# Kernel tuning notes

Measured on AMD Instinct MI355X. Metric: run time of the kernel, lower is better.

## Reference

```python
import jax, jax.numpy as jnp
import numpy as np

N_PTS = 2_000_000
N_VOX = 500_000
N_EMB = 1_000_000
EMBED_DIM = 16


def _interp_offset():
    # 8 corners of the unit cube, same order as torch.meshgrid([0,1]*3) -> reshape(-1,3)
    o = jnp.array([0.0, 1.0], dtype=jnp.float32)
    return jnp.stack(jnp.meshgrid(o, o, o, indexing='ij'), axis=-1).reshape(-1, 3)  # [8,3]


def setup_inputs() -> dict:
    key = jax.random.key(0)
    k1, k2, k3, k4, k5 = jax.random.split(key, 5)
    pts = jax.random.uniform(k1, (N_PTS, 3), dtype=jnp.float32)
    p2v_idx = jax.random.randint(k2, (N_PTS,), 0, N_VOX, dtype=jnp.int64 if jax.config.jax_enable_x64 else jnp.int32)
    embeddings = jax.random.normal(k3, (N_EMB, EMBED_DIM), dtype=jnp.float32) * (EMBED_DIM ** -0.5)
    center_points = jax.random.uniform(k4, (N_VOX, 3), dtype=jnp.float32)
    center2corner = jax.random.randint(k5, (N_VOX, 8), 0, N_EMB, dtype=jnp.int64 if jax.config.jax_enable_x64 else jnp.int32)
    voxel_size = jnp.ones((1,), dtype=jnp.float32)
    return {"pts": pts, "p2v_idx": p2v_idx, "embeddings": embeddings,
            "center_points": center_points, "center2corner": center2corner,
            "voxel_size": voxel_size}


def reference(pts, p2v_idx, embeddings, center_points, center2corner, voxel_size):
    offset = _interp_offset()                      # [8,3]
    cp = center_points[p2v_idx]                    # [N,3]   gather voxel centers
    cidx = center2corner[p2v_idx]                  # [N,8]   gather corner indices
    emb = embeddings[cidx]                         # [N,8,D] gather corner embeddings
    # relative position inside voxel, in [0,1]
    p = (pts - cp) / voxel_size + 0.5              # [N,3]
    p = p[:, None, :]                              # [N,1,3]
    # trilinear weights: prod over xyz of (p if corner==1 else 1-p)
    r = jnp.prod(p * offset + (1.0 - p) * (1.0 - offset), axis=-1)  # [N,8]
    return jnp.einsum('nc,ncd->nd', r, emb)        # [N,D]
```

## Files before the change

kernel.cpp:

```cpp
#include <hip/hip_runtime.h>


typedef float v4f __attribute__((ext_vector_type(4)));


__global__ void k_init_gbase(unsigned* __restrict__ gbase, int NB, unsigned CAP) {
    int i = blockIdx.x * blockDim.x + threadIdx.x;
    if (i < NB) gbase[i] = (unsigned)i * CAP;
}

__global__ __launch_bounds__(1024) void k_bucket(
    const int*   __restrict__ p2v,
    const float* __restrict__ pts,
    unsigned*    __restrict__ gbase,
    unsigned*    __restrict__ vA,
    v4f*         __restrict__ recA,
    int N, int NB)
{
    __shared__ unsigned cnt[512];
    __shared__ unsigned cur[512];
    const int tid = threadIdx.x;
    const int i0 = (blockIdx.x * 1024 + tid) * 8;

    for (int b = tid; b < NB; b += 1024) cnt[b] = 0u;
    __syncthreads();

    int vv[8];
    const bool full = (i0 + 7 < N);
    if (full) {
        const int4 a = *(const int4*)(p2v + i0);
        const int4 b4 = *(const int4*)(p2v + i0 + 4);
        vv[0]=a.x; vv[1]=a.y; vv[2]=a.z; vv[3]=a.w;
        vv[4]=b4.x; vv[5]=b4.y; vv[6]=b4.z; vv[7]=b4.w;
        #pragma unroll
        for (int k = 0; k < 8; ++k) atomicAdd(&cnt[vv[k] >> 11], 1u);
    } else {
        for (int k = 0; k < 8; ++k)
            if (i0 + k < N) { vv[k] = p2v[i0 + k]; atomicAdd(&cnt[vv[k] >> 11], 1u); }
    }
    __syncthreads();

    for (int b = tid; b < NB; b += 1024) {
        const unsigned c = cnt[b];
        cur[b] = c ? atomicAdd(&gbase[b], c) : 0u;
    }
    __syncthreads();

    if (full) {
        const v4f* p4 = (const v4f*)pts;
        const size_t fb = (size_t)3 * (size_t)(i0 >> 2);
        const v4f f0 = p4[fb], f1 = p4[fb+1], f2 = p4[fb+2];
        const v4f f3 = p4[fb+3], f4 = p4[fb+4], f5 = p4[fb+5];
        const float xs[8] = {f0.x, f0.w, f1.z, f2.y, f3.x, f3.w, f4.z, f5.y};
        const float ys[8] = {f0.y, f1.x, f1.w, f2.z, f3.y, f4.x, f4.w, f5.z};
        const float zs[8] = {f0.z, f1.y, f2.x, f2.w, f3.z, f4.y, f5.x, f5.w};
        #pragma unroll
        for (int k = 0; k < 8; ++k) {
            const unsigned pos = atomicAdd(&cur[vv[k] >> 11], 1u);
            v4f r; r.x = xs[k]; r.y = ys[k]; r.z = zs[k]; r.w = __int_as_float(i0 + k);
            recA[pos] = r;
            vA[pos] = (unsigned)vv[k];
        }
    } else {
        for (int k = 0; k < 8; ++k) {
            const int i = i0 + k;
            if (i >= N) break;
            const unsigned pos = atomicAdd(&cur[vv[k] >> 11], 1u);
            v4f r;
            r.x = pts[3*(size_t)i]; r.y = pts[3*(size_t)i+1]; r.z = pts[3*(size_t)i+2];
            r.w = __int_as_float(i);
            recA[pos] = r;
            vA[pos] = (unsigned)vv[k];
        }
    }
}

__global__ __launch_bounds__(256) void k_scan_nb(const unsigned* __restrict__ gbase,
                                                 unsigned* __restrict__ bo,
                                                 int NB, unsigned CAP) {
    __shared__ unsigned tsum[256];
    const int tid = threadIdx.x;
    const int i0 = tid * 2;
    const unsigned c0 = (i0     < NB) ? gbase[i0]     - (unsigned)i0       * CAP : 0u;
    const unsigned c1 = (i0 + 1 < NB) ? gbase[i0 + 1] - (unsigned)(i0 + 1) * CAP : 0u;
    tsum[tid] = c0 + c1; __syncthreads();
    for (int off = 1; off < 256; off <<= 1) {
        unsigned x = tsum[tid];
        unsigned y = (tid >= off) ? tsum[tid - off] : 0u;
        __syncthreads();
        tsum[tid] = x + y;
        __syncthreads();
    }
    const unsigned prefix = (tid > 0) ? tsum[tid - 1] : 0u;
    if (i0     < NB) bo[i0]     = prefix;
    if (i0 + 1 < NB) bo[i0 + 1] = prefix + c0;
}

__global__ __launch_bounds__(1024) void k_binsort(
    const unsigned* __restrict__ gbase,
    const unsigned* __restrict__ bo,
    const unsigned* __restrict__ vA,
    const v4f*      __restrict__ recA,
    unsigned*       __restrict__ vsort,
    v4f*            __restrict__ rec,
    unsigned CAP)
{
    __shared__ unsigned h[2048];
    __shared__ unsigned tsum[1024];
    const int b   = blockIdx.x;
    const int tid = threadIdx.x;
    const unsigned in0   = (unsigned)b * CAP;
    const unsigned cntb  = gbase[b] - in0;
    const unsigned obase = bo[b];
    const unsigned vbase = (unsigned)b << 11;

    h[tid] = 0u; h[tid + 1024] = 0u;
    __syncthreads();

    for (unsigned j = tid; j < cntb; j += 1024)
        atomicAdd(&h[vA[in0 + j] - vbase], 1u);
    __syncthreads();

    const unsigned a0 = h[2 * tid];
    const unsigned a1 = h[2 * tid + 1];
    tsum[tid] = a0 + a1; __syncthreads();
    for (int off = 1; off < 1024; off <<= 1) {
        unsigned x = tsum[tid];
        unsigned y = (tid >= off) ? tsum[tid - off] : 0u;
        __syncthreads();
        tsum[tid] = x + y;
        __syncthreads();
    }
    const unsigned pre = (tid > 0) ? tsum[tid - 1] : 0u;
    h[2 * tid]     = pre;
    h[2 * tid + 1] = pre + a0;
    __syncthreads();

    for (unsigned j = tid; j < cntb; j += 1024) {
        const unsigned v = vA[in0 + j];
        const unsigned r = atomicAdd(&h[v - vbase], 1u);
        const unsigned pos = obase + r;
        vsort[pos] = v;
        rec[pos] = recA[in0 + j];
    }
}

__global__ __launch_bounds__(256) void k_main(
    const unsigned* __restrict__ vsort, const v4f* __restrict__ rec,
    const float* __restrict__ emb,
    const float* __restrict__ cp,
    const int*   __restrict__ c2c,
    const float* __restrict__ vox,
    float*       __restrict__ out,
    int n0, int n1)
{
    const int t = blockIdx.x * blockDim.x + threadIdx.x;
    const int n = n0 + (t >> 2);
    const int q = t & 3;
    if (n >= n1) return;

    const unsigned v = vsort[n];
    const v4f r = rec[n];
    const int orig = __float_as_int(r.w);

    const int4* c4 = (const int4*)(c2c + 8 * (size_t)v);
    const int4 ci0 = c4[0];
    const int4 ci1 = c4[1];
    const int cidx[8] = {ci0.x, ci0.y, ci0.z, ci0.w, ci1.x, ci1.y, ci1.z, ci1.w};

    v4f e[8];
    #pragma unroll
    for (int c = 0; c < 8; ++c) {
        e[c] = *(const v4f*)(emb + 16 * (size_t)cidx[c] + 4 * q);
    }

    const float inv_vs = 1.0f / vox[0];
    const float* cpp = cp + 3 * (size_t)v;
    const float px = (r.x - cpp[0]) * inv_vs + 0.5f;
    const float py = (r.y - cpp[1]) * inv_vs + 0.5f;
    const float pz = (r.z - cpp[2]) * inv_vs + 0.5f;
    const float wx[2] = {1.0f - px, px};
    const float wy[2] = {1.0f - py, py};
    const float wz[2] = {1.0f - pz, pz};

    v4f acc = (v4f)(0.0f);
    #pragma unroll
    for (int c = 0; c < 8; ++c) {
        const float w = wx[(c >> 2) & 1] * wy[(c >> 1) & 1] * wz[c & 1];
        acc.x = fmaf(w, e[c].x, acc.x);
        acc.y = fmaf(w, e[c].y, acc.y);
        acc.z = fmaf(w, e[c].z, acc.z);
        acc.w = fmaf(w, e[c].w, acc.w);
    }

    __builtin_nontemporal_store(acc, (v4f*)(out + 16 * (size_t)orig + 4 * q));
}


__global__ void k_zero(unsigned* __restrict__ hist, int n) {
    int i = blockIdx.x * blockDim.x + threadIdx.x;
    if (i < n) hist[i] = 0u;
}

__global__ __launch_bounds__(256) void k_hist_rank(const int* __restrict__ p2v,
                                                   unsigned* __restrict__ hist,
                                                   unsigned* __restrict__ rank, int N) {
    const int base = (blockIdx.x * blockDim.x + threadIdx.x) * 8;
    if (base + 7 < N) {
        const int4 a = *(const int4*)(p2v + base);
        const int4 b = *(const int4*)(p2v + base + 4);
        const unsigned r0 = atomicAdd(&hist[a.x], 1u);
        const unsigned r1 = atomicAdd(&hist[a.y], 1u);
        const unsigned r2 = atomicAdd(&hist[a.z], 1u);
        const unsigned r3 = atomicAdd(&hist[a.w], 1u);
        const unsigned r4 = atomicAdd(&hist[b.x], 1u);
        const unsigned r5 = atomicAdd(&hist[b.y], 1u);
        const unsigned r6 = atomicAdd(&hist[b.z], 1u);
        const unsigned r7 = atomicAdd(&hist[b.w], 1u);
        uint4 o0; o0.x = r0; o0.y = r1; o0.z = r2; o0.w = r3;
        uint4 o1; o1.x = r4; o1.y = r5; o1.z = r6; o1.w = r7;
        *(uint4*)(rank + base)     = o0;
        *(uint4*)(rank + base + 4) = o1;
    } else {
        for (int k = 0; k < 8; ++k)
            if (base + k < N) rank[base + k] = atomicAdd(&hist[p2v[base + k]], 1u);
    }
}

__global__ __launch_bounds__(256) void k_scan_blocks(unsigned* __restrict__ hist,
                                                     unsigned* __restrict__ bsums, int nbins) {
    __shared__ unsigned tsum[256];
    const int tid = threadIdx.x;
    const int i0 = blockIdx.x * 1024 + tid * 4;
    unsigned v[4]; unsigned s = 0;
    #pragma unroll
    for (int k = 0; k < 4; ++k) {
        unsigned c = (i0 + k < nbins) ? hist[i0 + k] : 0u;
        v[k] = s; s += c;
    }
    tsum[tid] = s; __syncthreads();
    for (int off = 1; off < 256; off <<= 1) {
        unsigned x = tsum[tid];
        unsigned y = (tid >= off) ? tsum[tid - off] : 0u;
        __syncthreads();
        tsum[tid] = x + y;
        __syncthreads();
    }
    unsigned prefix = (tid > 0) ? tsum[tid - 1] : 0u;
    #pragma unroll
    for (int k = 0; k < 4; ++k) {
        if (i0 + k < nbins) hist[i0 + k] = prefix + v[k];
    }
    if (tid == 255) bsums[blockIdx.x] = tsum[255];
}

__global__ __launch_bounds__(256) void k_scan_sums(unsigned* __restrict__ bsums, int nb) {
    __shared__ unsigned tsum[256];
    const int tid = threadIdx.x;
    const int i0 = tid * 4;
    unsigned v[4]; unsigned s = 0;
    #pragma unroll
    for (int k = 0; k < 4; ++k) {
        unsigned c = (i0 + k < nb) ? bsums[i0 + k] : 0u;
        v[k] = s; s += c;
    }
    tsum[tid] = s; __syncthreads();
    for (int off = 1; off < 256; off <<= 1) {
        unsigned x = tsum[tid];
        unsigned y = (tid >= off) ? tsum[tid - off] : 0u;
        __syncthreads();
        tsum[tid] = x + y;
        __syncthreads();
    }
    unsigned prefix = (tid > 0) ? tsum[tid - 1] : 0u;
    #pragma unroll
    for (int k = 0; k < 4; ++k) {
        if (i0 + k < nb) bsums[i0 + k] = prefix + v[k];
    }
}

__global__ __launch_bounds__(256) void k_place(
    const float* __restrict__ pts,
    const int*   __restrict__ p2v,
    const unsigned* __restrict__ rank,
    const unsigned* __restrict__ hist,
    const unsigned* __restrict__ bsums,
    unsigned* __restrict__ vsort,
    v4f*      __restrict__ rec,
    int N)
{
    const int base = (blockIdx.x * blockDim.x + threadIdx.x) * 4;
    if (base + 3 < N) {
        const int4  v4r = *(const int4*)(p2v + base);
        const uint4 r4  = *(const uint4*)(rank + base);
        const v4f* p4 = (const v4f*)pts;
        const size_t f0i = (size_t)(3 * (base >> 2));
        const v4f f0 = p4[f0i];
        const v4f f1 = p4[f0i + 1];
        const v4f f2 = p4[f0i + 2];

        const unsigned pos0 = hist[v4r.x] + bsums[((unsigned)v4r.x) >> 10] + r4.x;
        const unsigned pos1 = hist[v4r.y] + bsums[((unsigned)v4r.y) >> 10] + r4.y;
        const unsigned pos2 = hist[v4r.z] + bsums[((unsigned)v4r.z) >> 10] + r4.z;
        const unsigned pos3 = hist[v4r.w] + bsums[((unsigned)v4r.w) >> 10] + r4.w;

        vsort[pos0] = (unsigned)v4r.x;
        vsort[pos1] = (unsigned)v4r.y;
        vsort[pos2] = (unsigned)v4r.z;
        vsort[pos3] = (unsigned)v4r.w;

        v4f a;
        a.x = f0.x; a.y = f0.y; a.z = f0.z; a.w = __int_as_float(base + 0);
        rec[pos0] = a;
        a.x = f0.w; a.y = f1.x; a.z = f1.y; a.w = __int_as_float(base + 1);
        rec[pos1] = a;
        a.x = f1.z; a.y = f1.w; a.z = f2.x; a.w = __int_as_float(base + 2);
        rec[pos2] = a;
        a.x = f2.y; a.y = f2.z; a.z = f2.w; a.w = __int_as_float(base + 3);
        rec[pos3] = a;
    } else {
        for (int k = 0; k < 4; ++k) {
            const int i = base + k;
            if (i >= N) break;
            const int v = p2v[i];
            const unsigned pos = hist[v] + bsums[((unsigned)v) >> 10] + rank[i];
            vsort[pos] = (unsigned)v;
            v4f r;
            r.x = pts[3 * (size_t)i + 0];
            r.y = pts[3 * (size_t)i + 1];
            r.z = pts[3 * (size_t)i + 2];
            r.w = __int_as_float(i);
            rec[pos] = r;
        }
    }
}

__global__ __launch_bounds__(256) void k_direct(
    const float* __restrict__ pts, const int* __restrict__ p2v,
    const float* __restrict__ emb, const float* __restrict__ cp,
    const int* __restrict__ c2c, const float* __restrict__ vox,
    float* __restrict__ out, int N)
{
    const int t = blockIdx.x * blockDim.x + threadIdx.x;
    const int n = t >> 2, q = t & 3;
    if (n >= N) return;
    const int v = p2v[n];
    const int4* c4 = (const int4*)(c2c + 8 * (size_t)v);
    const int4 ci0 = c4[0], ci1 = c4[1];
    const int cidx[8] = {ci0.x, ci0.y, ci0.z, ci0.w, ci1.x, ci1.y, ci1.z, ci1.w};
    v4f e[8];
    #pragma unroll
    for (int c = 0; c < 8; ++c) e[c] = *(const v4f*)(emb + 16 * (size_t)cidx[c] + 4 * q);
    const float inv_vs = 1.0f / vox[0];
    const float* pp = pts + 3 * (size_t)n;
    const float* cpp = cp + 3 * (size_t)v;
    const float px = (pp[0] - cpp[0]) * inv_vs + 0.5f;
    const float py = (pp[1] - cpp[1]) * inv_vs + 0.5f;
    const float pz = (pp[2] - cpp[2]) * inv_vs + 0.5f;
    const float wx[2] = {1.0f - px, px};
    const float wy[2] = {1.0f - py, py};
    const float wz[2] = {1.0f - pz, pz};
    v4f acc = (v4f)(0.0f);
    #pragma unroll
    for (int c = 0; c < 8; ++c) {
        const float w = wx[(c >> 2) & 1] * wy[(c >> 1) & 1] * wz[c & 1];
        acc.x = fmaf(w, e[c].x, acc.x); acc.y = fmaf(w, e[c].y, acc.y);
        acc.z = fmaf(w, e[c].z, acc.z); acc.w = fmaf(w, e[c].w, acc.w);
    }
    __builtin_nontemporal_store(acc, (v4f*)(out + 4 * (size_t)t));
}


extern "C" void kernel_launch(void* const* d_in, const int* in_sizes, int n_in,
                              void* d_out, int out_size, void* d_ws, size_t ws_size,
                              hipStream_t stream) {
    const float* pts = (const float*)d_in[0];
    const int*   p2v = (const int*)d_in[1];
    const float* emb = (const float*)d_in[2];
    const float* cp  = (const float*)d_in[3];
    const int*   c2c = (const int*)d_in[4];
    const float* vox = (const float*)d_in[5];
    float*       out = (float*)d_out;

    const int N  = in_sizes[1];
    const int NV = in_sizes[4] / 8;
    const int block = 256;

    const int NB = (NV + 2047) >> 11;
    if (NB >= 1 && NB <= 512) {
        const unsigned CAP = (unsigned)(N / NB) + 2048u;
        const size_t off_gbase = 0;
        const size_t off_bo    = 4096;
        const size_t off_vA    = 8192;
        const size_t sz_vA     = (size_t)NB * CAP * 4u;
        const size_t off_recA  = (off_vA + sz_vA + 255u) & ~(size_t)255u;
        const size_t sz_recA   = (size_t)NB * CAP * 16u;
        const size_t off_vsF   = (off_recA + sz_recA + 255u) & ~(size_t)255u;
        const size_t off_recF  = (off_vsF + (size_t)N * 4u + 255u) & ~(size_t)255u;
        const size_t need_fast = off_recF + (size_t)N * 16u;

        if (ws_size >= need_fast) {
            unsigned* gbase = (unsigned*)((char*)d_ws + off_gbase);
            unsigned* bo    = (unsigned*)((char*)d_ws + off_bo);
            unsigned* vA    = (unsigned*)((char*)d_ws + off_vA);
            v4f*      recA  = (v4f*)((char*)d_ws + off_recA);
            unsigned* vsort = (unsigned*)((char*)d_ws + off_vsF);
            v4f*      rec   = (v4f*)((char*)d_ws + off_recF);

            k_init_gbase<<<(NB + block - 1) / block, block, 0, stream>>>(gbase, NB, CAP);
            k_bucket<<<(N + 8191) / 8192, 1024, 0, stream>>>(p2v, pts, gbase, vA, recA, N, NB);
            k_scan_nb<<<1, block, 0, stream>>>(gbase, bo, NB, CAP);
            k_binsort<<<NB, 1024, 0, stream>>>(gbase, bo, vA, recA, vsort, rec, CAP);

            const long long th = 4LL * N;
            k_main<<<(int)((th + block - 1) / block), block, 0, stream>>>(
                vsort, rec, emb, cp, c2c, vox, out, 0, N);
            return;
        }
    }

    {
        const size_t MB = 1024u * 1024u;
        const size_t off_hist  = 0;
        const size_t off_bsums = 2u * MB;
        const size_t off_rank  = 4u * MB;
        const size_t off_vsort = 12u * MB;
        const size_t off_rec   = 20u * MB;
        const size_t need = off_rec + (size_t)N * 16u;

        if (ws_size >= need) {
            unsigned* hist  = (unsigned*)((char*)d_ws + off_hist);
            unsigned* bsums = (unsigned*)((char*)d_ws + off_bsums);
            unsigned* rank  = (unsigned*)((char*)d_ws + off_rank);
            unsigned* vsort = (unsigned*)((char*)d_ws + off_vsort);
            v4f*      rec   = (v4f*)((char*)d_ws + off_rec);

            const int nscan = (NV + 1023) / 1024;

            k_zero<<<(NV + block - 1) / block, block, 0, stream>>>(hist, NV);
            k_hist_rank<<<(N + block * 8 - 1) / (block * 8), block, 0, stream>>>(p2v, hist, rank, N);
            k_scan_blocks<<<nscan, 256, 0, stream>>>(hist, bsums, NV);
            k_scan_sums<<<1, 256, 0, stream>>>(bsums, nscan);
            k_place<<<(N + block * 4 - 1) / (block * 4), block, 0, stream>>>(
                pts, p2v, rank, hist, bsums, vsort, rec, N);

            const long long threads = 4LL * N;
            k_main<<<(int)((threads + block - 1) / block), block, 0, stream>>>(
                vsort, rec, emb, cp, c2c, vox, out, 0, N);
            return;
        }
    }

    {
        const long long threads = 4LL * N;
        k_direct<<<(int)((threads + block - 1) / block), block, 0, stream>>>(
            pts, p2v, emb, cp, c2c, vox, out, N);
    }
}
```

Measured before the change: 383.4 us.

## Drop per-bucket binsort and scan; compute directly from coarse bucket buffers

```diff
diff --git a/kernel.cpp b/kernel.cpp
--- a/kernel.cpp
+++ b/kernel.cpp
@@ -75,92 +75,35 @@
     }
 }
 
-__global__ __launch_bounds__(256) void k_scan_nb(const unsigned* __restrict__ gbase,
-                                                 unsigned* __restrict__ bo,
-                                                 int NB, unsigned CAP) {
-    __shared__ unsigned tsum[256];
-    const int tid = threadIdx.x;
-    const int i0 = tid * 2;
-    const unsigned c0 = (i0     < NB) ? gbase[i0]     - (unsigned)i0       * CAP : 0u;
-    const unsigned c1 = (i0 + 1 < NB) ? gbase[i0 + 1] - (unsigned)(i0 + 1) * CAP : 0u;
-    tsum[tid] = c0 + c1; __syncthreads();
-    for (int off = 1; off < 256; off <<= 1) {
-        unsigned x = tsum[tid];
-        unsigned y = (tid >= off) ? tsum[tid - off] : 0u;
-        __syncthreads();
-        tsum[tid] = x + y;
-        __syncthreads();
-    }
-    const unsigned prefix = (tid > 0) ? tsum[tid - 1] : 0u;
-    if (i0     < NB) bo[i0]     = prefix;
-    if (i0 + 1 < NB) bo[i0 + 1] = prefix + c0;
-}
-
-__global__ __launch_bounds__(1024) void k_binsort(
+__global__ __launch_bounds__(256) void k_main_b(
     const unsigned* __restrict__ gbase,
-    const unsigned* __restrict__ bo,
     const unsigned* __restrict__ vA,
     const v4f*      __restrict__ recA,
-    unsigned*       __restrict__ vsort,
-    v4f*            __restrict__ rec,
-    unsigned CAP)
-{
-    __shared__ unsigned h[2048];
-    __shared__ unsigned tsum[1024];
-    const int b   = blockIdx.x;
-    const int tid = threadIdx.x;
-    const unsigned in0   = (unsigned)b * CAP;
-    const unsigned cntb  = gbase[b] - in0;
-    const unsigned obase = bo[b];
-    const unsigned vbase = (unsigned)b << 11;
-
-    h[tid] = 0u; h[tid + 1024] = 0u;
-    __syncthreads();
-
-    for (unsigned j = tid; j < cntb; j += 1024)
-        atomicAdd(&h[vA[in0 + j] - vbase], 1u);
-    __syncthreads();
-
-    const unsigned a0 = h[2 * tid];
-    const unsigned a1 = h[2 * tid + 1];
-    tsum[tid] = a0 + a1; __syncthreads();
-    for (int off = 1; off < 1024; off <<= 1) {
-        unsigned x = tsum[tid];
-        unsigned y = (tid >= off) ? tsum[tid - off] : 0u;
-        __syncthreads();
-        tsum[tid] = x + y;
-        __syncthreads();
-    }
-    const unsigned pre = (tid > 0) ? tsum[tid - 1] : 0u;
-    h[2 * tid]     = pre;
-    h[2 * tid + 1] = pre + a0;
-    __syncthreads();
-
-    for (unsigned j = tid; j < cntb; j += 1024) {
-        const unsigned v = vA[in0 + j];
-        const unsigned r = atomicAdd(&h[v - vbase], 1u);
-        const unsigned pos = obase + r;
-        vsort[pos] = v;
-        rec[pos] = recA[in0 + j];
-    }
-}
-
-__global__ __launch_bounds__(256) void k_main(
-    const unsigned* __restrict__ vsort, const v4f* __restrict__ rec,
     const float* __restrict__ emb,
     const float* __restrict__ cp,
     const int*   __restrict__ c2c,
     const float* __restrict__ vox,
     float*       __restrict__ out,
-    int n0, int n1)
+    int NB)
 {
-    const int t = blockIdx.x * blockDim.x + threadIdx.x;
-    const int n = n0 + (t >> 2);
-    const int q = t & 3;
-    if (n >= n1) return;
-
-    const unsigned v = vsort[n];
-    const v4f r = rec[n];
+    const int bid = blockIdx.x;
+    const int x   = bid & 7;
+    const int t2  = bid >> 3;
+    const int c   = t2 >> 8;
+    const int j   = t2 & 255;
+    const int b   = (c << 3) | x;
+    if (b >= NB) return;
+
+    const unsigned base = (unsigned)b << 14;
+    const unsigned cntb = gbase[b] - base;
+    const unsigned local = (unsigned)(j << 6) + (threadIdx.x >> 2);
+    if (local >= cntb) return;
+
+    const unsigned n = base + local;
+    const int q = threadIdx.x & 3;
+
+    const unsigned v = vA[n];
+    const v4f r = recA[n];
     const int orig = __float_as_int(r.w);
 
     const int4* c4 = (const int4*)(c2c + 8 * (size_t)v);
@@ -170,8 +113,8 @@
 
     v4f e[8];
     #pragma unroll
-    for (int c = 0; c < 8; ++c) {
-        e[c] = *(const v4f*)(emb + 16 * (size_t)cidx[c] + 4 * q);
+    for (int cc = 0; cc < 8; ++cc) {
+        e[cc] = *(const v4f*)(emb + 16 * (size_t)cidx[cc] + 4 * q);
     }
 
     const float inv_vs = 1.0f / vox[0];
@@ -185,12 +128,12 @@
 
     v4f acc = (v4f)(0.0f);
     #pragma unroll
-    for (int c = 0; c < 8; ++c) {
-        const float w = wx[(c >> 2) & 1] * wy[(c >> 1) & 1] * wz[c & 1];
-        acc.x = fmaf(w, e[c].x, acc.x);
-        acc.y = fmaf(w, e[c].y, acc.y);
-        acc.z = fmaf(w, e[c].z, acc.z);
-        acc.w = fmaf(w, e[c].w, acc.w);
+    for (int cc = 0; cc < 8; ++cc) {
+        const float w = wx[(cc >> 2) & 1] * wy[(cc >> 1) & 1] * wz[cc & 1];
+        acc.x = fmaf(w, e[cc].x, acc.x);
+        acc.y = fmaf(w, e[cc].y, acc.y);
+        acc.z = fmaf(w, e[cc].z, acc.z);
+        acc.w = fmaf(w, e[cc].w, acc.w);
     }
 
     __builtin_nontemporal_store(acc, (v4f*)(out + 16 * (size_t)orig + 4 * q));
@@ -335,6 +278,57 @@
     }
 }
 
+__global__ __launch_bounds__(256) void k_main(
+    const unsigned* __restrict__ vsort, const v4f* __restrict__ rec,
+    const float* __restrict__ emb,
+    const float* __restrict__ cp,
+    const int*   __restrict__ c2c,
+    const float* __restrict__ vox,
+    float*       __restrict__ out,
+    int n0, int n1)
+{
+    const int t = blockIdx.x * blockDim.x + threadIdx.x;
+    const int n = n0 + (t >> 2);
+    const int q = t & 3;
+    if (n >= n1) return;
+
+    const unsigned v = vsort[n];
+    const v4f r = rec[n];
+    const int orig = __float_as_int(r.w);
+
+    const int4* c4 = (const int4*)(c2c + 8 * (size_t)v);
+    const int4 ci0 = c4[0];
+    const int4 ci1 = c4[1];
+    const int cidx[8] = {ci0.x, ci0.y, ci0.z, ci0.w, ci1.x, ci1.y, ci1.z, ci1.w};
+
+    v4f e[8];
+    #pragma unroll
+    for (int c = 0; c < 8; ++c) {
+        e[c] = *(const v4f*)(emb + 16 * (size_t)cidx[c] + 4 * q);
+    }
+
+    const float inv_vs = 1.0f / vox[0];
+    const float* cpp = cp + 3 * (size_t)v;
+    const float px = (r.x - cpp[0]) * inv_vs + 0.5f;
+    const float py = (r.y - cpp[1]) * inv_vs + 0.5f;
+    const float pz = (r.z - cpp[2]) * inv_vs + 0.5f;
+    const float wx[2] = {1.0f - px, px};
+    const float wy[2] = {1.0f - py, py};
+    const float wz[2] = {1.0f - pz, pz};
+
+    v4f acc = (v4f)(0.0f);
+    #pragma unroll
+    for (int c = 0; c < 8; ++c) {
+        const float w = wx[(c >> 2) & 1] * wy[(c >> 1) & 1] * wz[c & 1];
+        acc.x = fmaf(w, e[c].x, acc.x);
+        acc.y = fmaf(w, e[c].y, acc.y);
+        acc.z = fmaf(w, e[c].z, acc.z);
+        acc.w = fmaf(w, e[c].w, acc.w);
+    }
+
+    __builtin_nontemporal_store(acc, (v4f*)(out + 16 * (size_t)orig + 4 * q));
+}
+
 __global__ __launch_bounds__(256) void k_direct(
     const float* __restrict__ pts, const int* __restrict__ p2v,
     const float* __restrict__ emb, const float* __restrict__ cp,
@@ -387,34 +381,26 @@
     const int block = 256;
 
     const int NB = (NV + 2047) >> 11;
-    if (NB >= 1 && NB <= 512) {
-        const unsigned CAP = (unsigned)(N / NB) + 2048u;
+    const unsigned CAP = 16384u;
+    if (NB >= 1 && NB <= 512 && (unsigned)(N / NB) + 2048u <= CAP) {
         const size_t off_gbase = 0;
-        const size_t off_bo    = 4096;
         const size_t off_vA    = 8192;
         const size_t sz_vA     = (size_t)NB * CAP * 4u;
         const size_t off_recA  = (off_vA + sz_vA + 255u) & ~(size_t)255u;
-        const size_t sz_recA   = (size_t)NB * CAP * 16u;
-        const size_t off_vsF   = (off_recA + sz_recA + 255u) & ~(size_t)255u;
-        const size_t off_recF  = (off_vsF + (size_t)N * 4u + 255u) & ~(size_t)255u;
-        const size_t need_fast = off_recF + (size_t)N * 16u;
+        const size_t need_fast = off_recA + (size_t)NB * CAP * 16u;
 
         if (ws_size >= need_fast) {
             unsigned* gbase = (unsigned*)((char*)d_ws + off_gbase);
-            unsigned* bo    = (unsigned*)((char*)d_ws + off_bo);
             unsigned* vA    = (unsigned*)((char*)d_ws + off_vA);
             v4f*      recA  = (v4f*)((char*)d_ws + off_recA);
-            unsigned* vsort = (unsigned*)((char*)d_ws + off_vsF);
-            v4f*      rec   = (v4f*)((char*)d_ws + off_recF);
 
             k_init_gbase<<<(NB + block - 1) / block, block, 0, stream>>>(gbase, NB, CAP);
             k_bucket<<<(N + 8191) / 8192, 1024, 0, stream>>>(p2v, pts, gbase, vA, recA, N, NB);
-            k_scan_nb<<<1, block, 0, stream>>>(gbase, bo, NB, CAP);
-            k_binsort<<<NB, 1024, 0, stream>>>(gbase, bo, vA, recA, vsort, rec, CAP);
-
-            const long long th = 4LL * N;
-            k_main<<<(int)((th + block - 1) / block), block, 0, stream>>>(
-                vsort, rec, emb, cp, c2c, vox, out, 0, N);
+
+            const int classes = (NB + 7) >> 3;
+            const int grid = 8 * classes * 256;
+            k_main_b<<<grid, block, 0, stream>>>(
+                gbase, vA, recA, emb, cp, c2c, vox, out, NB);
             return;
         }
     }
```

Result: no change. 388.8 us (+1.4%).

## Map main-kernel blocks to buckets interleaved across XCDs for L2 locality

Applied to the files above, without the earlier changes.

```diff
diff --git a/kernel.cpp b/kernel.cpp
--- a/kernel.cpp
+++ b/kernel.cpp
@@ -140,24 +140,36 @@
         const unsigned v = vA[in0 + j];
         const unsigned r = atomicAdd(&h[v - vbase], 1u);
         const unsigned pos = obase + r;
-        vsort[pos] = v;
-        rec[pos] = recA[in0 + j];
-    }
-}
-
-__global__ __launch_bounds__(256) void k_main(
+        __builtin_nontemporal_store(v, vsort + pos);
+        __builtin_nontemporal_store(recA[in0 + j], rec + pos);
+    }
+}
+
+__global__ __launch_bounds__(256) void k_main_a(
+    const unsigned* __restrict__ gbase,
+    const unsigned* __restrict__ bo,
     const unsigned* __restrict__ vsort, const v4f* __restrict__ rec,
     const float* __restrict__ emb,
     const float* __restrict__ cp,
     const int*   __restrict__ c2c,
     const float* __restrict__ vox,
     float*       __restrict__ out,
-    int n0, int n1)
+    int NB, unsigned CAP)
 {
-    const int t = blockIdx.x * blockDim.x + threadIdx.x;
-    const int n = n0 + (t >> 2);
-    const int q = t & 3;
-    if (n >= n1) return;
+    const int bid = blockIdx.x;
+    const int x   = bid & 7;
+    const int t2  = bid >> 3;
+    const int c   = t2 >> 8;
+    const int j   = t2 & 255;
+    const int b   = (c << 3) | x;
+    if (b >= NB) return;
+
+    const unsigned cntb  = gbase[b] - (unsigned)b * CAP;
+    const unsigned local = (unsigned)(j << 6) + (threadIdx.x >> 2);
+    if (local >= cntb) return;
+
+    const unsigned n = bo[b] + local;
+    const int q = threadIdx.x & 3;
 
     const unsigned v = vsort[n];
     const v4f r = rec[n];
@@ -170,8 +182,8 @@
 
     v4f e[8];
     #pragma unroll
-    for (int c = 0; c < 8; ++c) {
-        e[c] = *(const v4f*)(emb + 16 * (size_t)cidx[c] + 4 * q);
+    for (int cc = 0; cc < 8; ++cc) {
+        e[cc] = *(const v4f*)(emb + 16 * (size_t)cidx[cc] + 4 * q);
     }
 
     const float inv_vs = 1.0f / vox[0];
@@ -185,12 +197,12 @@
 
     v4f acc = (v4f)(0.0f);
     #pragma unroll
-    for (int c = 0; c < 8; ++c) {
-        const float w = wx[(c >> 2) & 1] * wy[(c >> 1) & 1] * wz[c & 1];
-        acc.x = fmaf(w, e[c].x, acc.x);
-        acc.y = fmaf(w, e[c].y, acc.y);
-        acc.z = fmaf(w, e[c].z, acc.z);
-        acc.w = fmaf(w, e[c].w, acc.w);
+    for (int cc = 0; cc < 8; ++cc) {
+        const float w = wx[(cc >> 2) & 1] * wy[(cc >> 1) & 1] * wz[cc & 1];
+        acc.x = fmaf(w, e[cc].x, acc.x);
+        acc.y = fmaf(w, e[cc].y, acc.y);
+        acc.z = fmaf(w, e[cc].z, acc.z);
+        acc.w = fmaf(w, e[cc].w, acc.w);
     }
 
     __builtin_nontemporal_store(acc, (v4f*)(out + 16 * (size_t)orig + 4 * q));
@@ -335,6 +347,57 @@
     }
 }
 
+__global__ __launch_bounds__(256) void k_main(
+    const unsigned* __restrict__ vsort, const v4f* __restrict__ rec,
+    const float* __restrict__ emb,
+    const float* __restrict__ cp,
+    const int*   __restrict__ c2c,
+    const float* __restrict__ vox,
+    float*       __restrict__ out,
+    int n0, int n1)
+{
+    const int t = blockIdx.x * blockDim.x + threadIdx.x;
+    const int n = n0 + (t >> 2);
+    const int q = t & 3;
+    if (n >= n1) return;
+
+    const unsigned v = vsort[n];
+    const v4f r = rec[n];
+    const int orig = __float_as_int(r.w);
+
+    const int4* c4 = (const int4*)(c2c + 8 * (size_t)v);
+    const int4 ci0 = c4[0];
+    const int4 ci1 = c4[1];
+    const int cidx[8] = {ci0.x, ci0.y, ci0.z, ci0.w, ci1.x, ci1.y, ci1.z, ci1.w};
+
+    v4f e[8];
+    #pragma unroll
+    for (int c = 0; c < 8; ++c) {
+        e[c] = *(const v4f*)(emb + 16 * (size_t)cidx[c] + 4 * q);
+    }
+
+    const float inv_vs = 1.0f / vox[0];
+    const float* cpp = cp + 3 * (size_t)v;
+    const float px = (r.x - cpp[0]) * inv_vs + 0.5f;
+    const float py = (r.y - cpp[1]) * inv_vs + 0.5f;
+    const float pz = (r.z - cpp[2]) * inv_vs + 0.5f;
+    const float wx[2] = {1.0f - px, px};
+    const float wy[2] = {1.0f - py, py};
+    const float wz[2] = {1.0f - pz, pz};
+
+    v4f acc = (v4f)(0.0f);
+    #pragma unroll
+    for (int c = 0; c < 8; ++c) {
+        const float w = wx[(c >> 2) & 1] * wy[(c >> 1) & 1] * wz[c & 1];
+        acc.x = fmaf(w, e[c].x, acc.x);
+        acc.y = fmaf(w, e[c].y, acc.y);
+        acc.z = fmaf(w, e[c].z, acc.z);
+        acc.w = fmaf(w, e[c].w, acc.w);
+    }
+
+    __builtin_nontemporal_store(acc, (v4f*)(out + 16 * (size_t)orig + 4 * q));
+}
+
 __global__ __launch_bounds__(256) void k_direct(
     const float* __restrict__ pts, const int* __restrict__ p2v,
     const float* __restrict__ emb, const float* __restrict__ cp,
@@ -387,8 +450,8 @@
     const int block = 256;
 
     const int NB = (NV + 2047) >> 11;
-    if (NB >= 1 && NB <= 512) {
-        const unsigned CAP = (unsigned)(N / NB) + 2048u;
+    const unsigned CAP = 16384u;
+    if (NB >= 1 && NB <= 512 && (unsigned)(N / NB) + 2048u <= CAP) {
         const size_t off_gbase = 0;
         const size_t off_bo    = 4096;
         const size_t off_vA    = 8192;
@@ -412,9 +475,10 @@
             k_scan_nb<<<1, block, 0, stream>>>(gbase, bo, NB, CAP);
             k_binsort<<<NB, 1024, 0, stream>>>(gbase, bo, vA, recA, vsort, rec, CAP);
 
-            const long long th = 4LL * N;
-            k_main<<<(int)((th + block - 1) / block), block, 0, stream>>>(
-                vsort, rec, emb, cp, c2c, vox, out, 0, N);
+            const int classes = (NB + 7) >> 3;
+            const int grid = classes * 256 * 8;
+            k_main_a<<<grid, block, 0, stream>>>(
+                gbase, bo, vsort, rec, emb, cp, c2c, vox, out, NB, CAP);
             return;
         }
     }
```

Result: slower. 483.5 us (+26.1%).
